# Kernel tuning notes

Hardware: AMD Instinct MI355X
Metric: run time of the kernel (lower is better)

Reference implementation:

```python
import jax, jax.numpy as jnp
import numpy as np

N, P, F, E = 4096, 512, 4096, 65536
FN, FE = 32, 32
H, C = 4, 64
D = H * C
HL = 64
LMAX, LFMAX = 256, 16


def _bn(x, g, b):
    m = x.mean(0)
    v = jnp.mean((x - m) ** 2, 0)
    return (x - m) / jnp.sqrt(v + 1e-5) * g + b


def _gat(x, src, dst, eattr, W, We, asrc, adst, aedge, bias):
    # PyG GATConv with edge_dim: self-loops appended with fill_value='mean' edge attrs
    n = x.shape[0]
    cnt = jax.ops.segment_sum(jnp.ones((eattr.shape[0],), eattr.dtype), dst, n)
    sums = jax.ops.segment_sum(eattr, dst, n)
    loop_attr = jnp.where(cnt[:, None] > 0, sums / jnp.maximum(cnt, 1.0)[:, None], 0.0)
    loops = jnp.arange(n, dtype=src.dtype)
    s2 = jnp.concatenate([src, loops])
    d2 = jnp.concatenate([dst, loops])
    ea = jnp.concatenate([eattr, loop_attr], 0)
    h = (x @ W).reshape(n, H, C)
    e = (ea @ We).reshape(-1, H, C)
    logits = jax.nn.leaky_relu((h * asrc).sum(-1)[s2] + (h * adst).sum(-1)[d2] + (e * aedge).sum(-1), 0.2)
    mx = jax.ops.segment_max(logits, d2, n)
    w = jnp.exp(logits - mx[d2])
    alpha = w / jax.ops.segment_sum(w, d2, n)[d2]  # softmax over incoming edges per dst
    out = jax.ops.segment_sum(h[s2] * alpha[:, :, None], d2, n).reshape(n, D) + bias
    return out, s2, d2, alpha


def _lstm(seq, Wih, Whh, bih, bhh):
    # torch single-layer batch_first LSTM; gate order i,f,g,o
    B = seq.shape[0]
    hid = Whh.shape[1]
    def step(carry, xt):
        hp, cp = carry
        z = xt @ Wih.T + hp @ Whh.T + bih + bhh
        i, f, g, o = jnp.split(z, 4, axis=-1)
        c = jax.nn.sigmoid(f) * cp + jax.nn.sigmoid(i) * jnp.tanh(g)
        hh = jax.nn.sigmoid(o) * jnp.tanh(c)
        return (hh, c), hh
    init = (jnp.zeros((B, hid), seq.dtype), jnp.zeros((B, hid), seq.dtype))
    _, ys = jax.lax.scan(step, init, seq.transpose(1, 0, 2))
    return ys.transpose(1, 0, 2)


def _pack(x, mask_f, max_len):
    # scatter node ids into [S, max_len] slots (cumsum positions), then gather x
    mask = mask_f > 0.5
    n, S = mask.shape
    lengths = mask.sum(0)
    pos = jnp.cumsum(mask, 0) - 1
    slot = jnp.where(mask, jnp.arange(S)[None, :] * max_len + pos, S * max_len)
    node_ids = jnp.broadcast_to(jnp.arange(n, dtype=jnp.int32)[:, None], (n, S))
    buf = jnp.zeros(S * max_len + 1, jnp.int32).at[slot.reshape(-1)].set(node_ids.reshape(-1))
    nfs = buf[: S * max_len].reshape(S, max_len)
    valid = jnp.arange(max_len)[None, :] < lengths[:, None]
    seq = jnp.where(valid[:, :, None], x[nfs], 0.0)
    return seq, lengths


def _node_seq(x, mask_f, max_len, Wih, Whh, bih, bhh):
    seq, lengths = _pack(x, mask_f, max_len)
    out = _lstm(seq, Wih, Whh, bih, bhh)
    return out[jnp.arange(seq.shape[0]), lengths - 1]


def _splice(x, src_f, snk_f, emap, alpha, max_len, Wih, Whh, bih, bhh):
    # pair k-th source True with k-th sink True in row-major flatten order (torch masked-select semantics)
    src_m = src_f > 0.5
    snk_m = snk_f > 0.5
    n, S = src_m.shape
    lengths = src_m.sum(0)
    pos = jnp.cumsum(src_m, 0) - 1
    node_ids = jnp.broadcast_to(jnp.arange(n, dtype=jnp.int32)[:, None], (n, S)).reshape(-1)
    srcf = src_m.reshape(-1)
    snkf = snk_m.reshape(-1)
    total = n * S
    rank_snk = jnp.cumsum(snkf) - 1
    snk_by_rank = jnp.zeros(total + 1, jnp.int32).at[jnp.where(snkf, rank_snk, total)].set(node_ids)
    paired = snk_by_rank[jnp.cumsum(srcf) - 1]
    slot = jnp.where(src_m, jnp.arange(S)[None, :] * max_len + pos, S * max_len).reshape(-1)
    sbuf = jnp.zeros(S * max_len + 1, jnp.int32).at[slot].set(node_ids)
    tbuf = jnp.zeros(S * max_len + 1, jnp.int32).at[slot].set(paired)
    sn = sbuf[: S * max_len].reshape(S, max_len)
    tn = tbuf[: S * max_len].reshape(S, max_len)
    att = alpha[emap[sn * n + tn]]  # [S, T, H]
    se = (x[sn].reshape(S, max_len, H, C) * att[..., None]).reshape(S, max_len, D)
    te = (x[tn].reshape(S, max_len, H, C) * att[..., None]).reshape(S, max_len, D)
    emb = jnp.concatenate([se, te], -1)
    valid = jnp.arange(max_len)[None, :] < lengths[:, None]
    emb = jnp.where(valid[:, :, None], emb, 0.0)
    out = _lstm(emb, Wih, Whh, bih, bhh)
    return out[jnp.arange(S), lengths - 1]


def _compat(paths, frags):
    # mismatch-count reformulation of ((path==frag) | ~span_mask).all(0): exact for 0/1 masks
    n = paths.shape[0]
    relevance = (paths.T @ frags) > 0.0
    fb = frags > 0.5
    fs = jnp.argmax(fb, 0)
    fe = n - 1 - jnp.argmax(fb[::-1], 0)
    r = jnp.arange(n)[:, None]
    fmask = ((r >= fs[None, :]) & (r <= fe[None, :])).astype(paths.dtype)
    mism = frags.T @ (1.0 - paths) + (fmask - frags).T @ paths  # [F, P]
    compat = mism.T == 0.0
    pos = (relevance & compat).astype(paths.dtype)
    neg = (relevance & (~compat)).astype(paths.dtype)
    return pos, neg


def reference(x, edge_index, edge_attr, candidate_paths, candidate_paths_source, candidate_paths_sink, path_abundance, fragments, bn_x_g, bn_x_b, bn_e_g, bn_e_b, gat0_W, gat0_We, gat0_asrc, gat0_adst, gat0_aedge, gat0_bias, gat1_W, gat1_We, gat1_asrc, gat1_adst, gat1_aedge, gat1_bias, node_Wih, node_Whh, node_bih, node_bhh, splice_Wih, splice_Whh, splice_bih, splice_bhh, frag_Wih, frag_Whh, frag_bih, frag_bhh, fc1_W, fc1_b, fc2_W, fc2_b):
    xn = _bn(x, bn_x_g, bn_x_b)
    ea = _bn(edge_attr, bn_e_g, bn_e_b)
    src, dst = edge_index[0], edge_index[1]
    h, _, _, _ = _gat(xn, src, dst, ea, gat0_W, gat0_We, gat0_asrc, gat0_adst, gat0_aedge, gat0_bias)
    h = jax.nn.elu(h)
    h, s2, d2, alpha = _gat(h, src, dst, ea, gat1_W, gat1_We, gat1_asrc, gat1_adst, gat1_aedge, gat1_bias)
    h = jax.nn.elu(h)
    n = h.shape[0]
    emap = jnp.zeros(n * n, jnp.int32).at[s2 * n + d2].set(jnp.arange(s2.shape[0], dtype=jnp.int32))
    node_emb = _node_seq(h, candidate_paths, LMAX, node_Wih, node_Whh, node_bih, node_bhh)
    splice_emb = _splice(h, candidate_paths_source, candidate_paths_sink, emap, alpha, LMAX, splice_Wih, splice_Whh, splice_bih, splice_bhh)
    path_emb = jnp.concatenate([node_emb, splice_emb, path_abundance[:, None]], -1)
    frag_emb = _node_seq(h, fragments, LFMAX, frag_Wih, frag_Whh, frag_bih, frag_bhh)
    pos, neg = _compat(candidate_paths, fragments)
    combined = jnp.concatenate([path_emb, pos @ frag_emb, neg @ frag_emb], -1)
    score = jax.nn.relu(combined @ fc1_W.T + fc1_b) @ fc2_W.T + fc2_b
    return jax.nn.sigmoid(score[:, 0])


def setup_inputs():
    rng = np.random.default_rng(0)
    keys = jax.random.split(jax.random.key(0), 40)
    idx = np.arange(N)[:, None]
    ps = rng.integers(0, N - LMAX, P)
    pl = rng.integers(16, LMAX + 1, P)
    cp = ((idx >= ps) & (idx < ps + pl)).astype(np.float32)
    cps = ((idx >= ps) & (idx < ps + pl - 1)).astype(np.float32)
    cpk = ((idx >= ps + 1) & (idx < ps + pl)).astype(np.float32)
    fst = rng.integers(0, N - LFMAX, F)
    fl = rng.integers(2, LFMAX + 1, F)
    fr = ((idx >= fst) & (idx < fst + fl)).astype(np.float32)
    # unique off-diagonal edges; first N-1 are consecutive (n, n+1) so splice lookups hit real edges
    consec = np.arange(N - 1) * (N - 1) + np.arange(N - 1)
    r_rand = rng.choice(N * (N - 1), size=E, replace=False)
    r = np.concatenate([consec, np.setdiff1d(r_rand, consec)])[:E]
    esrc = r // (N - 1)
    rem = r % (N - 1)
    edst = rem + (rem >= esrc)
    edge_index = jnp.asarray(np.stack([esrc, edst]).astype(np.int32))
    g = lambda k, s, sc=0.1: jax.random.normal(keys[k], s, jnp.float32) * sc
    return dict(
        x=g(0, (N, FN), 1.0),
        edge_index=edge_index,
        edge_attr=g(1, (E, FE), 1.0),
        candidate_paths=jnp.asarray(cp),
        candidate_paths_source=jnp.asarray(cps),
        candidate_paths_sink=jnp.asarray(cpk),
        path_abundance=jax.random.uniform(keys[2], (P,)),
        fragments=jnp.asarray(fr),
        bn_x_g=jnp.ones((FN,)), bn_x_b=jnp.zeros((FN,)),
        bn_e_g=jnp.ones((FE,)), bn_e_b=jnp.zeros((FE,)),
        gat0_W=g(3, (FN, D)), gat0_We=g(4, (FE, D)), gat0_asrc=g(5, (H, C)), gat0_adst=g(6, (H, C)), gat0_aedge=g(7, (H, C)), gat0_bias=g(8, (D,)),
        gat1_W=g(9, (D, D)), gat1_We=g(10, (FE, D)), gat1_asrc=g(11, (H, C)), gat1_adst=g(12, (H, C)), gat1_aedge=g(13, (H, C)), gat1_bias=g(14, (D,)),
        node_Wih=g(15, (4 * HL, D)), node_Whh=g(16, (4 * HL, HL)), node_bih=g(17, (4 * HL,)), node_bhh=g(18, (4 * HL,)),
        splice_Wih=g(19, (4 * HL, 2 * D)), splice_Whh=g(20, (4 * HL, HL)), splice_bih=g(21, (4 * HL,)), splice_bhh=g(22, (4 * HL,)),
        frag_Wih=g(23, (4 * HL, D)), frag_Whh=g(24, (4 * HL, HL)), frag_bih=g(25, (4 * HL,)), frag_bhh=g(26, (4 * HL,)),
        fc1_W=g(27, (HL, 4 * HL + 1)), fc1_b=g(28, (HL,)), fc2_W=g(29, (1, HL)), fc2_b=g(30, (1,)),
    )
```

## Files before the change

### kernel.cpp

```cpp
#include <hip/hip_runtime.h>


constexpr int cN = 4096, cP = 512, cE = 65536, cF = 4096, cM = cE + cN;
constexpr int cLMAX = 256;

typedef float f32x4 __attribute__((ext_vector_type(4)));
typedef unsigned int u32;
typedef u32 u32x4 __attribute__((ext_vector_type(4)));

#define DEV __device__ __forceinline__
DEV float sigf(float x)  { return 1.f / (1.f + __expf(-x)); }
DEV float tanhx(float x) { return 2.f / (1.f + __expf(-2.f * x)) - 1.f; }
DEV float eluf(float x)  { return x > 0.f ? x : (__expf(x) - 1.f); }
DEV float lrelu(float x) { return x > 0.f ? x : 0.2f * x; }
DEV u32   b16rne(float f){ u32 u = __float_as_uint(f); u += 0x7fff + ((u >> 16) & 1); return u >> 16; }
DEV float lobf(u32 d)    { return __uint_as_float(d << 16); }
DEV float hibf(u32 d)    { return __uint_as_float(d & 0xffff0000u); }

#define LBAR() asm volatile("s_waitcnt lgkmcnt(0)\n\ts_barrier" ::: "memory")


DEV void dev_bn_stats(const float* __restrict__ x, long rows,
                      float* sums, float* sumsq, int bid, int nb,
                      float* ls, float* lq) {
  int tid = threadIdx.x;
  long total = rows * 32;
  float s = 0.f, q = 0.f;
  for (long i = (long)bid * 256 + tid; i < total; i += (long)nb * 256) {
    float v = x[i]; s += v; q += v * v;
  }
  ls[tid] = s; lq[tid] = q; __syncthreads();
  if (tid < 32) {
    float S = 0.f, Q = 0.f;
    for (int j = tid; j < 256; j += 32) { S += ls[j]; Q += lq[j]; }
    atomicAdd(&sums[tid], S); atomicAdd(&sumsq[tid], Q);
  }
}

DEV void dev_prep_small(const float* We0, const float* ae0,
                        const float* We1, const float* ae1,
                        const float* nbih, const float* nbhh,
                        const float* fbih, const float* fbhh,
                        const float* sbih, const float* sbhh,
                        float* q0, float* q1, float* nbo, float* fbo, float* sbo) {
  int tid = threadIdx.x;
  if (tid < 128) {
    int k = tid >> 2, hh = tid & 3;
    float s0 = 0.f, s1 = 0.f;
    for (int c = 0; c < 64; c++) {
      s0 += We0[k * 256 + hh * 64 + c] * ae0[hh * 64 + c];
      s1 += We1[k * 256 + hh * 64 + c] * ae1[hh * 64 + c];
    }
    q0[tid] = s0; q1[tid] = s1;
  }
  nbo[tid] = nbih[tid] + nbhh[tid];
  fbo[tid] = fbih[tid] + fbhh[tid];
  sbo[tid] = sbih[tid] + sbhh[tid];
}

DEV void dev_pack(const float* WN, const float* WS, const float* WF,
                  u32* pN, u32* pS, u32* pF, int bid) {
  int gid = bid * 256 + threadIdx.x;
  int mat = gid >> 13, idx = gid & 8191;
  const float* w = (mat == 0) ? WN : (mat == 1 ? WS : WF);
  u32* d = (mat == 0) ? pN : (mat == 1 ? pS : pF);
  float a = w[idx * 2], b = w[idx * 2 + 1];
  d[idx] = b16rne(a) | (b16rne(b) << 16);
}

DEV void dev_deg_count(const int* __restrict__ ei, int* deg, int bid) {
  int m = bid * 256 + threadIdx.x;
  if (m < cE) atomicAdd(&deg[ei[cE + m]], 1);
}

DEV void dev_bn_apply(const float* __restrict__ x, const float* __restrict__ e,
                      const float* bnst, const float* xg, const float* xb,
                      const float* eg, const float* eb,
                      float* xn, float* ea, int bid, int nb, float* sc) {
  int tid = threadIdx.x;
  if (tid < 32) {
    float m = bnst[tid] / (float)cN;
    float v = bnst[32 + tid] / (float)cN - m * m;
    float s = xg[tid] * rsqrtf(v + 1e-5f);
    sc[tid] = s; sc[32 + tid] = xb[tid] - m * s;
  } else if (tid < 64) {
    int c = tid - 32;
    float m = bnst[64 + c] / (float)cE;
    float v = bnst[96 + c] / (float)cE - m * m;
    float s = eg[c] * rsqrtf(v + 1e-5f);
    sc[64 + c] = s; sc[96 + c] = eb[c] - m * s;
  }
  __syncthreads();
  long t1 = (long)cN * 32, t2 = t1 + (long)cE * 32;
  for (long i = (long)bid * 256 + tid; i < t2; i += (long)nb * 256) {
    if (i < t1) { int c = (int)(i & 31); xn[i] = x[i] * sc[c] + sc[32 + c]; }
    else { long j = i - t1; int c = (int)(j & 31); ea[j] = e[j] * sc[64 + c] + sc[96 + c]; }
  }
}

DEV void dev_scan_offsets(const int* __restrict__ deg, int* offs,
                          int* tsum, int* tpre) {
  int tid = threadIdx.x;
  int base = tid * 16, s = 0; int loc[16];
  for (int i = 0; i < 16; i++) { loc[i] = s; s += deg[base + i] + 1; }
  tsum[tid] = s; __syncthreads();
  if (tid == 0) { int r = 0; for (int j = 0; j < 256; j++) { tpre[j] = r; r += tsum[j]; } tpre[256] = r; }
  __syncthreads();
  for (int i = 0; i < 16; i++) offs[base + i] = tpre[tid] + loc[i];
  if (tid == 255) offs[cN] = tpre[256];
}

DEV void dev_intervals(const float* __restrict__ cp, const float* __restrict__ cps,
                       const float* __restrict__ fr,
                       int* p_s, int* p_e, int* s_s, int* s_e,
                       int* f_s, int* f_e, int bid, int nb) {
  const long T1 = (long)cN * cP, T2 = 2 * T1, T3 = T2 + (long)cN * cF;
  for (long i = (long)bid * 256 + threadIdx.x; i < T3; i += (long)nb * 256) {
    if (i < T1) {
      if (cp[i] > 0.5f) { int col = (int)(i % cP), row = (int)(i / cP);
        atomicMin(&p_s[col], row); atomicMax(&p_e[col], row); }
    } else if (i < T2) {
      long j = i - T1;
      if (cps[j] > 0.5f) { int col = (int)(j % cP), row = (int)(j / cP);
        atomicMin(&s_s[col], row); atomicMax(&s_e[col], row); }
    } else {
      long j = i - T2;
      if (fr[j] > 0.5f) { int col = (int)(j % cF), row = (int)(j / cF);
        atomicMin(&f_s[col], row); atomicMax(&f_e[col], row); }
    }
  }
}

DEV void dev_csr_fill(const int* __restrict__ ei, const int* __restrict__ offs,
                      int* cursor, int* eids, int bid) {
  int m = bid * 256 + threadIdx.x;
  if (m < cE) {
    int d = ei[cE + m];
    int pos = atomicAdd(&cursor[d], 1);
    eids[offs[d] + pos] = m;
  } else if (m < cM) {
    int n = m - cE;
    int pos = atomicAdd(&cursor[n], 1);
    eids[offs[n] + pos] = m;
  }
}

DEV void dev_loop_attr(const float* __restrict__ ea, const int* __restrict__ offs,
                       const int* __restrict__ eids,
                       const float* q0, const float* q1,
                       float* es0, float* es1, int n, float* la) {
  int tid = threadIdx.x;
  int o0 = offs[n], o1 = offs[n + 1];
  if (tid < 32) {
    float s = 0.f; int cnt = 0;
    for (int x = o0; x < o1; x++) {
      int eid = eids[x];
      if (eid < cE) { s += ea[(size_t)eid * 32 + tid]; cnt++; }
    }
    la[tid] = cnt > 0 ? s / (float)cnt : 0.f;
  }
  __syncthreads();
  if (tid < 8) {
    int hh = tid & 3;
    const float* q = (tid < 4) ? q0 : q1;
    float s = 0.f;
    for (int k = 0; k < 32; k++) s += la[k] * q[k * 4 + hh];
    ((tid < 4) ? es0 : es1)[(size_t)(cE + n) * 4 + hh] = s;
  }
}

DEV void dev_node_scores(const float* __restrict__ h, const float* __restrict__ asrc,
                         const float* __restrict__ adst, float* ssrc, float* sdst,
                         int bid) {
  int idx = bid * 256 + threadIdx.x;
  if (idx >= cN * 4) return;
  int n = idx >> 2, hh = idx & 3;
  float s1 = 0.f, s2 = 0.f;
  const float* hr = h + (size_t)n * 256 + hh * 64;
  const float* a1 = asrc + hh * 64;
  const float* a2 = adst + hh * 64;
  for (int c = 0; c < 64; c++) { float v = hr[c]; s1 += v * a1[c]; s2 += v * a2[c]; }
  ssrc[idx] = s1; sdst[idx] = s2;
}

DEV void dev_es_edges(const float* __restrict__ ea, const float* __restrict__ q,
                      float* es, int bid) {
  int m = bid * 256 + threadIdx.x;
  if (m >= cE) return;
  float a0 = 0.f, a1 = 0.f, a2 = 0.f, a3 = 0.f;
  const float4* r4 = (const float4*)(ea + (size_t)m * 32);
#pragma unroll
  for (int k4 = 0; k4 < 8; k4++) {
    float4 v = r4[k4];
    int k = k4 * 4;
    a0 += v.x * q[k * 4] + v.y * q[(k + 1) * 4] + v.z * q[(k + 2) * 4] + v.w * q[(k + 3) * 4];
    a1 += v.x * q[k * 4 + 1] + v.y * q[(k + 1) * 4 + 1] + v.z * q[(k + 2) * 4 + 1] + v.w * q[(k + 3) * 4 + 1];
    a2 += v.x * q[k * 4 + 2] + v.y * q[(k + 1) * 4 + 2] + v.z * q[(k + 2) * 4 + 2] + v.w * q[(k + 3) * 4 + 2];
    a3 += v.x * q[k * 4 + 3] + v.y * q[(k + 1) * 4 + 3] + v.z * q[(k + 2) * 4 + 3] + v.w * q[(k + 3) * 4 + 3];
  }
  float* o = es + (size_t)m * 4;
  o[0] = a0; o[1] = a1; o[2] = a2; o[3] = a3;
}

template <bool NT, bool PERM>
DEV void dev_gemm(const float* __restrict__ A, const float* __restrict__ B,
                  const float* __restrict__ bias, float* __restrict__ C,
                  int M, int Nc, int K, int lda, int ldb, int ldc,
                  int bid, float (*As)[68], float (*Bs)[68]) {
  int nb = Nc / 64;
  int bx = bid % nb, by = bid / nb;
  int j0 = bx * 64, i0 = by * 64;
  int tid = threadIdx.x, tx = tid % 16, ty = tid / 16;
  float acc[4][4] = {};

  float ar[4], br[4];
  auto loadA = [&](int k0, float* r4) {
#pragma unroll
    for (int p = 0; p < 4; p++) {
      int l = p * 256 + tid; int r = l >> 4, c = l & 15;
      r4[p] = A[(size_t)(i0 + r) * lda + k0 + c];
    }
  };
  auto loadB = [&](int k0, float* r4) {
    if (NT) {
#pragma unroll
      for (int p = 0; p < 4; p++) {
        int l = p * 256 + tid; int r = l >> 4, c = l & 15;
        r4[p] = B[(size_t)(j0 + r) * ldb + k0 + c];
      }
    } else {
#pragma unroll
      for (int p = 0; p < 4; p++) {
        int l = p * 256 + tid; int j = l & 63, c = l >> 6;
        r4[p] = B[(size_t)(k0 + c) * ldb + j0 + j];
      }
    }
  };

  loadA(0, ar); loadB(0, br);
  for (int k0 = 0; k0 < K; k0 += 16) {
#pragma unroll
    for (int p = 0; p < 4; p++) {
      int l = p * 256 + tid;
      As[l & 15][l >> 4] = ar[p];
    }
    if (NT) {
#pragma unroll
      for (int p = 0; p < 4; p++) {
        int l = p * 256 + tid;
        Bs[l & 15][l >> 4] = br[p];
      }
    } else {
#pragma unroll
      for (int p = 0; p < 4; p++) {
        int l = p * 256 + tid;
        Bs[l >> 6][l & 63] = br[p];
      }
    }
    __syncthreads();
    if (k0 + 16 < K) { loadA(k0 + 16, ar); loadB(k0 + 16, br); }
#pragma unroll
    for (int kk = 0; kk < 16; kk++) {
      f32x4 a4 = *(const f32x4*)&As[kk][ty * 4];
      f32x4 b4 = *(const f32x4*)&Bs[kk][tx * 4];
      float av[4] = {a4.x, a4.y, a4.z, a4.w};
      float bv[4] = {b4.x, b4.y, b4.z, b4.w};
#pragma unroll
      for (int u = 0; u < 4; u++)
#pragma unroll
        for (int v = 0; v < 4; v++) acc[u][v] = fmaf(av[u], bv[v], acc[u][v]);
    }
    __syncthreads();
  }
#pragma unroll
  for (int u = 0; u < 4; u++)
#pragma unroll
    for (int v = 0; v < 4; v++) {
      int i = i0 + ty * 4 + u, j = j0 + tx * 4 + v;
      float r = acc[u][v] + (bias ? bias[j] : 0.f);
      int jj = PERM ? (((j & 63) << 2) | (j >> 6)) : j;
      C[(size_t)i * ldc + jj] = r;
    }
}

DEV void dev_gemm_g(const float* __restrict__ hf, const float* __restrict__ sWih,
                    float* __restrict__ Gp, int bid,
                    float (*As)[68], float (*Bs)[68]) {
  int hh = bid & 3, jt = (bid >> 2) & 3, mt = bid >> 4;
  int i0 = mt * 64, j0 = jt * 64;
  int tid = threadIdx.x, tx = tid & 15, ty = tid >> 4;
  float acc[4][4] = {};

  float ar[4], br[4];
  auto loadT = [&](int k0, float* ra, float* rb) {
    int second = (k0 >= 64);
    int kb = hh * 64 + (k0 & 63);
#pragma unroll
    for (int p = 0; p < 4; p++) {
      int l = p * 256 + tid; int r = l >> 4, c = l & 15;
      int row = i0 + r + second;
      ra[p] = (row < cN) ? hf[(size_t)row * 256 + kb + c] : 0.f;
      rb[p] = sWih[(size_t)(j0 + r) * 512 + second * 256 + kb + c];
    }
  };

  loadT(0, ar, br);
  for (int k0 = 0; k0 < 128; k0 += 16) {
#pragma unroll
    for (int p = 0; p < 4; p++) {
      int l = p * 256 + tid;
      As[l & 15][l >> 4] = ar[p];
      Bs[l & 15][l >> 4] = br[p];
    }
    __syncthreads();
    if (k0 + 16 < 128) loadT(k0 + 16, ar, br);
#pragma unroll
    for (int kk = 0; kk < 16; kk++) {
      f32x4 a4 = *(const f32x4*)&As[kk][ty * 4];
      f32x4 b4 = *(const f32x4*)&Bs[kk][tx * 4];
      float av[4] = {a4.x, a4.y, a4.z, a4.w};
      float bv[4] = {b4.x, b4.y, b4.z, b4.w};
#pragma unroll
      for (int u = 0; u < 4; u++)
#pragma unroll
        for (int v = 0; v < 4; v++) acc[u][v] = fmaf(av[u], bv[v], acc[u][v]);
    }
    __syncthreads();
  }
#pragma unroll
  for (int u = 0; u < 4; u++)
#pragma unroll
    for (int v = 0; v < 4; v++) {
      int i = i0 + ty * 4 + u, j = j0 + tx * 4 + v;
      int g = j >> 6, un = j & 63;
      Gp[(size_t)i * 1024 + un * 16 + g * 4 + hh] = acc[u][v];
    }
}

DEV void dev_att_prep(const int* __restrict__ s_s, const int* __restrict__ s_e,
                      const int* __restrict__ offs, const int* __restrict__ eids,
                      const int* __restrict__ ei, const float* __restrict__ alpha1,
                      float* att, int bid) {
  int idx = bid * 256 + threadIdx.x;
  int s = idx / cLMAX, t = idx % cLMAX;
  int ss = s_s[s], len = s_e[s] - ss + 1;
  float4 a4 = make_float4(0.f, 0.f, 0.f, 0.f);
  if (t < len) {
    int a = ss + t, b = a + 1;
    int found = 0;
    for (int x = offs[b]; x < offs[b + 1]; x++) {
      int eid = eids[x];
      int src = (eid < cE) ? ei[eid] : b;
      if (src == a) { found = eid; break; }
    }
    a4 = *(const float4*)&alpha1[(size_t)found * 4];
  }
  *(float4*)&att[(size_t)idx * 4] = a4;
}


__global__ void init_k(float* bnst, int* deg, int* cursor,
                       int* p_s, int* p_e, int* s_s, int* s_e,
                       int* f_s, int* f_e) {
  int i = blockIdx.x * 256 + threadIdx.x;
  if (i < 128) bnst[i] = 0.f;
  if (i < cN) { deg[i] = 0; cursor[i] = 0; f_s[i] = 0x7fffffff; f_e[i] = -1; }
  if (i < cP) { p_s[i] = 0x7fffffff; p_e[i] = -1; s_s[i] = 0x7fffffff; s_e[i] = -1; }
}

__global__ __launch_bounds__(256) void setup_k(
    const float* x, const float* eattr, const int* ei,
    const float* We0, const float* ae0, const float* We1, const float* ae1,
    const float* nbih, const float* nbhh, const float* fbih, const float* fbhh,
    const float* sbih, const float* sbhh,
    const float* WhhN, const float* WhhS, const float* WhhF,
    float* bnst, int* deg,
    float* q0, float* q1, float* nbo, float* fbo, float* sbo,
    u32* pN, u32* pS, u32* pF) {
  __shared__ float ls[256], lq[256];
  int b = blockIdx.x;
  if (b < 64)        dev_bn_stats(x, cN, bnst, bnst + 32, b, 64, ls, lq);
  else if (b < 320)  dev_bn_stats(eattr, cE, bnst + 64, bnst + 96, b - 64, 256, ls, lq);
  else if (b < 576)  dev_deg_count(ei, deg, b - 320);
  else if (b == 576) dev_prep_small(We0, ae0, We1, ae1, nbih, nbhh, fbih, fbhh,
                                    sbih, sbhh, q0, q1, nbo, fbo, sbo);
  else               dev_pack(WhhN, WhhS, WhhF, pN, pS, pF, b - 577);
}

__global__ __launch_bounds__(256) void mid_k(
    const float* x, const float* eattr, const float* bnst,
    const float* xg, const float* xb, const float* eg, const float* eb,
    float* xn, float* ea, const int* deg, int* offs,
    const float* cp, const float* cps, const float* fr,
    int* p_s, int* p_e, int* s_s, int* s_e, int* f_s, int* f_e) {
  __shared__ int ts[256], tp[257];
  int b = blockIdx.x;
  if (b < 2048)       dev_bn_apply(x, eattr, bnst, xg, xb, eg, eb, xn, ea, b, 2048, (float*)ts);
  else if (b == 2048) dev_scan_offsets(deg, offs, ts, tp);
  else                dev_intervals(cp, cps, fr, p_s, p_e, s_s, s_e, f_s, f_e, b - 2049, 4096);
}

__global__ __launch_bounds__(256) void k3(
    const float* xn, const float* g0W, float* h0,
    const int* ei, const int* offs, int* cursor, int* eids) {
  __shared__ __align__(16) float As[16][68], Bs[16][68];
  int b = blockIdx.x;
  if (b < 256) dev_gemm<false, false>(xn, g0W, nullptr, h0, 4096, 256, 32, 32, 256, 256, b, As, Bs);
  else         dev_csr_fill(ei, offs, cursor, eids, b - 256);
}

__global__ __launch_bounds__(256) void k4(
    const float* ea, const int* offs, const int* eids,
    const float* q0, const float* q1, float* es0, float* es1,
    const float* h0, const float* g0as, const float* g0ad,
    float* ssrc0, float* sdst0) {
  __shared__ float la[32];
  int b = blockIdx.x;
  if (b < 4096)      dev_loop_attr(ea, offs, eids, q0, q1, es0, es1, b, la);
  else if (b < 4160) dev_node_scores(h0, g0as, g0ad, ssrc0, sdst0, b - 4096);
  else               dev_es_edges(ea, q0, es0, b - 4160);
}

__global__ __launch_bounds__(256) void gat_agg(
    const float* __restrict__ hfeat, const float* __restrict__ ssrc,
    const float* __restrict__ sdst, const float* __restrict__ es,
    const int* __restrict__ offs, const int* __restrict__ eids,
    const int* __restrict__ ei, const float* __restrict__ bias,
    float* __restrict__ out, float* alpha_out) {
  int n = blockIdx.x, tid = threadIdx.x;
  __shared__ float l_lds[1024 * 4];
  __shared__ int s_lds[1024];
  __shared__ float red[4];
  int o0 = offs[n], o1 = offs[n + 1];
  int deg = o1 - o0; if (deg > 1024) deg = 1024;
  for (int idx = tid; idx < deg * 4; idx += 256) {
    int e = idx >> 2, hh = idx & 3;
    int eid = eids[o0 + e];
    int src = (eid < cE) ? ei[eid] : n;
    if (hh == 0) s_lds[e] = src;
    float lg = ssrc[src * 4 + hh] + sdst[n * 4 + hh] + es[(size_t)eid * 4 + hh];
    l_lds[idx] = lrelu(lg);
  }
  __syncthreads();
  if (tid < 4) {
    float mx = -1e30f;
    for (int e = 0; e < deg; e++) mx = fmaxf(mx, l_lds[e * 4 + tid]);
    float sm = 0.f;
    for (int e = 0; e < deg; e++) {
      float w = __expf(l_lds[e * 4 + tid] - mx);
      l_lds[e * 4 + tid] = w; sm += w;
    }
    red[tid] = 1.f / sm;
  }
  __syncthreads();
  for (int idx = tid; idx < deg * 4; idx += 256) {
    int e = idx >> 2, hh = idx & 3;
    float a = l_lds[idx] * red[hh];
    l_lds[idx] = a;
    if (alpha_out) { int eid = eids[o0 + e]; alpha_out[(size_t)eid * 4 + hh] = a; }
  }
  __syncthreads();
  int c = tid, hh = c >> 6;
  float acc = 0.f;
  for (int e = 0; e < deg; e++)
    acc = fmaf(l_lds[e * 4 + hh], hfeat[(size_t)s_lds[e] * 256 + c], acc);
  acc += bias[c];
  out[(size_t)n * 256 + c] = eluf(acc);
}

__global__ __launch_bounds__(256) void k6(const float* h0e, const float* g1W, float* h1) {
  __shared__ __align__(16) float As[16][68], Bs[16][68];
  dev_gemm<false, false>(h0e, g1W, nullptr, h1, 4096, 256, 256, 256, 256, 256, blockIdx.x, As, Bs);
}

__global__ __launch_bounds__(256) void k7(
    const float* h1, const float* g1as, const float* g1ad,
    float* ssrc1, float* sdst1, const float* ea, const float* q1, float* es1) {
  int b = blockIdx.x;
  if (b < 64) dev_node_scores(h1, g1as, g1ad, ssrc1, sdst1, b);
  else        dev_es_edges(ea, q1, es1, b - 64);
}

__global__ __launch_bounds__(256) void k9(
    const float* hf, const float* nWih, const float* nbo, float* Znp,
    const float* fWih, const float* fbo, float* Zfp,
    const float* sWih, float* Gp,
    const int* s_s, const int* s_e, const int* offs, const int* eids,
    const int* ei, const float* alpha1, float* att) {
  __shared__ __align__(16) float As[16][68], Bs[16][68];
  int b = blockIdx.x;
  if (b < 256)       dev_gemm<true, true>(hf, nWih, nbo, Znp, 4096, 256, 256, 256, 256, 256, b, As, Bs);
  else if (b < 512)  dev_gemm<true, true>(hf, fWih, fbo, Zfp, 4096, 256, 256, 256, 256, 256, b - 256, As, Bs);
  else if (b < 1536) dev_gemm_g(hf, sWih, Gp, b - 512, As, Bs);
  else               dev_att_prep(s_s, s_e, offs, eids, ei, alpha1, att, b - 1536);
}

__global__ __launch_bounds__(256, 4) void lstm_all(
    const float* __restrict__ Znp, const float* __restrict__ Zfp,
    const float* __restrict__ Gp, const float* __restrict__ att,
    const u32* __restrict__ wpN, const u32* __restrict__ wpS,
    const u32* __restrict__ wpF, const float* __restrict__ sbias,
    const int* __restrict__ p_s, const int* __restrict__ p_e,
    const int* __restrict__ s_s, const int* __restrict__ s_e,
    const int* __restrict__ f_s, const int* __restrict__ f_e,
    float* node_emb, float* spl_emb, float* frag_emb) {
  int b = blockIdx.x;
  int tid = threadIdx.x;
  int w = tid >> 6, lane = tid & 63;
  int g = lane & 3, ul = lane >> 2;
  int unit = w * 16 + ul;
  int role, sid;
  if (b < cP) { role = 0; sid = b; }
  else if (b < 2 * cP) { role = 1; sid = b - cP; }
  else { role = 2; sid = b - 2 * cP; }

  const u32* wp = (role == 0) ? wpN : (role == 1 ? wpS : wpF);
  const u32* wrow = wp + (size_t)(g * 64 + unit) * 32;
  u32 wd[32];
#pragma unroll
  for (int j = 0; j < 8; j++) {
    u32x4 v = *(const u32x4*)(wrow + 4 * j);
    wd[4 * j] = v.x; wd[4 * j + 1] = v.y; wd[4 * j + 2] = v.z; wd[4 * j + 3] = v.w;
  }
#pragma unroll
  for (int j = 0; j < 32; j++) asm volatile("" : "+v"(wd[j]));

  int start, len;
  if (role == 0) { start = p_s[sid]; len = p_e[sid] - start + 1; }
  else if (role == 1) { start = s_s[sid]; len = s_e[sid] - start + 1; }
  else { start = f_s[sid]; len = f_e[sid] - start + 1; }

  float sb = (role == 1) ? sbias[g * 64 + unit] : 0.f;

  const float* Zb = (role == 0) ? Znp : Zfp;
  __shared__ float hbuf[2][64];
  if (tid < 64) hbuf[0][tid] = 0.f;
  float cc = 0.f, h = 0.f;

  float zc = 0.f; f32x4 gc = {0.f, 0.f, 0.f, 0.f}, atc = gc;
  if (role == 1) {
    gc = *(const f32x4*)(Gp + (size_t)start * 1024 + tid * 4);
    atc = *(const f32x4*)(att + (size_t)sid * cLMAX * 4);
  } else {
    zc = Zb[(size_t)start * 256 + tid];
  }
  LBAR();

  for (int t = 0; t < len; t++) {
    int rb = t & 1;
    float zin = (role == 1)
        ? sb + atc.x * gc.x + atc.y * gc.y + atc.z * gc.z + atc.w * gc.w
        : zc;

    float znx = zc; f32x4 gnx = gc, atn = atc;
    if (t + 1 < len) {
      if (role == 1) {
        gnx = *(const f32x4*)(Gp + (size_t)(start + t + 1) * 1024 + tid * 4);
        atn = *(const f32x4*)(att + (size_t)(sid * cLMAX + t + 1) * 4);
      } else {
        znx = Zb[(size_t)(start + t + 1) * 256 + tid];
      }
    }

    float za = zin, zb2 = 0.f;
#pragma unroll
    for (int kc = 0; kc < 8; kc++) {
      f32x4 hv = *(const f32x4*)&hbuf[rb][4 * kc];
      u32 d0 = wd[2 * kc], d1 = wd[2 * kc + 1];
      za = fmaf(hv.x, lobf(d0), za); za = fmaf(hv.y, hibf(d0), za);
      za = fmaf(hv.z, lobf(d1), za); za = fmaf(hv.w, hibf(d1), za);
    }
#pragma unroll
    for (int kc = 8; kc < 16; kc++) {
      f32x4 hv = *(const f32x4*)&hbuf[rb][4 * kc];
      u32 d0 = wd[2 * kc], d1 = wd[2 * kc + 1];
      zb2 = fmaf(hv.x, lobf(d0), zb2); zb2 = fmaf(hv.y, hibf(d0), zb2);
      zb2 = fmaf(hv.z, lobf(d1), zb2); zb2 = fmaf(hv.w, hibf(d1), zb2);
    }
    float z = za + zb2;

    int base = lane & ~3;
    float zi = __shfl(z, base, 64);
    float zf = __shfl(z, base + 1, 64);
    float zg = __shfl(z, base + 2, 64);
    float zo = __shfl(z, base + 3, 64);

    float gi = sigf(zi), gf = sigf(zf), gg = tanhx(zg), go = sigf(zo);
    cc = gf * cc + gi * gg;
    h = go * tanhx(cc);

    if (g == 0) hbuf[rb ^ 1][unit] = h;
    LBAR();

    zc = znx; gc = gnx; atc = atn;
  }

  float* dst = (role == 0) ? node_emb : (role == 1 ? spl_emb : frag_emb);
  if (g == 0) dst[(size_t)sid * 64 + unit] = h;
}

__global__ __launch_bounds__(256) void score_final(
    const float* __restrict__ femb, const int* __restrict__ p_s,
    const int* __restrict__ p_e, const int* __restrict__ f_s,
    const int* __restrict__ f_e, const float* __restrict__ nemb,
    const float* __restrict__ semb, const float* __restrict__ abund,
    const float* __restrict__ fc1W, const float* __restrict__ fc1b,
    const float* __restrict__ fc2W, const float* __restrict__ fc2b,
    float* out) {
  int p = blockIdx.x, tid = threadIdx.x;
  __shared__ float cmb[257];
  __shared__ float accp[256], accn[256], r1[64];
  int ps = p_s[p], pe = p_e[p];
  int d = tid & 63, g = tid >> 6;
  float ap = 0.f, an = 0.f;
  for (int f = g; f < cF; f += 4) {
    int fs = f_s[f], fe = f_e[f];
    if (fs <= pe && fe >= ps) {
      float v = femb[(size_t)f * 64 + d];
      if (fs >= ps && fe <= pe) ap += v;
      else an += v;
    }
  }
  accp[tid] = ap; accn[tid] = an; __syncthreads();
  if (tid < 64) {
    cmb[tid] = nemb[(size_t)p * 64 + tid];
    cmb[64 + tid] = semb[(size_t)p * 64 + tid];
    cmb[129 + tid] = accp[tid] + accp[tid + 64] + accp[tid + 128] + accp[tid + 192];
    cmb[193 + tid] = accn[tid] + accn[tid + 64] + accn[tid + 128] + accn[tid + 192];
    if (tid == 0) cmb[128] = abund[p];
  }
  __syncthreads();
  if (tid < 64) {
    float s = fc1b[tid];
    for (int k = 0; k < 257; k++) s = fmaf(cmb[k], fc1W[tid * 257 + k], s);
    r1[tid] = s > 0.f ? s : 0.f;
  }
  __syncthreads();
  if (tid == 0) {
    float s = fc2b[0];
    for (int j = 0; j < 64; j++) s = fmaf(r1[j], fc2W[j], s);
    out[p] = 1.f / (1.f + __expf(-s));
  }
}

extern "C" void kernel_launch(void* const* d_in, const int* in_sizes, int n_in,
                              void* d_out, int out_size, void* d_ws, size_t ws_size,
                              hipStream_t stream) {
  (void)in_sizes; (void)n_in; (void)out_size; (void)ws_size;
  const float* x     = (const float*)d_in[0];
  const int*   ei    = (const int*)  d_in[1];
  const float* eattr = (const float*)d_in[2];
  const float* cp    = (const float*)d_in[3];
  const float* cps   = (const float*)d_in[4];
  const float* abund = (const float*)d_in[6];
  const float* frg   = (const float*)d_in[7];
  const float* bnxg  = (const float*)d_in[8];
  const float* bnxb  = (const float*)d_in[9];
  const float* bneg  = (const float*)d_in[10];
  const float* bneb  = (const float*)d_in[11];
  const float* g0W   = (const float*)d_in[12];
  const float* g0We  = (const float*)d_in[13];
  const float* g0as  = (const float*)d_in[14];
  const float* g0ad  = (const float*)d_in[15];
  const float* g0ae  = (const float*)d_in[16];
  const float* g0b   = (const float*)d_in[17];
  const float* g1W   = (const float*)d_in[18];
  const float* g1We  = (const float*)d_in[19];
  const float* g1as  = (const float*)d_in[20];
  const float* g1ad  = (const float*)d_in[21];
  const float* g1ae  = (const float*)d_in[22];
  const float* g1b   = (const float*)d_in[23];
  const float* nWih  = (const float*)d_in[24];
  const float* nWhh  = (const float*)d_in[25];
  const float* nbih  = (const float*)d_in[26];
  const float* nbhh  = (const float*)d_in[27];
  const float* sWih  = (const float*)d_in[28];
  const float* sWhh  = (const float*)d_in[29];
  const float* sbih  = (const float*)d_in[30];
  const float* sbhh  = (const float*)d_in[31];
  const float* fWih  = (const float*)d_in[32];
  const float* fWhh  = (const float*)d_in[33];
  const float* fbih  = (const float*)d_in[34];
  const float* fbhh  = (const float*)d_in[35];
  const float* fc1W  = (const float*)d_in[36];
  const float* fc1b  = (const float*)d_in[37];
  const float* fc2W  = (const float*)d_in[38];
  const float* fc2b  = (const float*)d_in[39];
  float* out = (float*)d_out;

  char* base = (char*)d_ws;
  size_t used = 0;
  auto alloc = [&](size_t nbytes) -> char* {
    char* p = base + used;
    used += (nbytes + 255) & ~(size_t)255;
    return p;
  };
  float* bnst   = (float*)alloc(128 * 4);
  float* q0     = (float*)alloc(128 * 4);
  float* q1     = (float*)alloc(128 * 4);
  float* nbo    = (float*)alloc(256 * 4);
  float* fbo    = (float*)alloc(256 * 4);
  float* sbo    = (float*)alloc(256 * 4);
  u32*   wpN    = (u32*)alloc(8192 * 4);
  u32*   wpS    = (u32*)alloc(8192 * 4);
  u32*   wpF    = (u32*)alloc(8192 * 4);
  float* xn     = (float*)alloc((size_t)cN * 32 * 4);
  float* eab    = (float*)alloc((size_t)cE * 32 * 4);
  float* h0     = (float*)alloc((size_t)cN * 256 * 4);
  float* h0e    = (float*)alloc((size_t)cN * 256 * 4);
  float* h1     = (float*)alloc((size_t)cN * 256 * 4);
  float* hf     = (float*)alloc((size_t)cN * 256 * 4);
  float* ssrc0  = (float*)alloc((size_t)cN * 4 * 4);
  float* sdst0  = (float*)alloc((size_t)cN * 4 * 4);
  float* ssrc1  = (float*)alloc((size_t)cN * 4 * 4);
  float* sdst1  = (float*)alloc((size_t)cN * 4 * 4);
  float* es0    = (float*)alloc((size_t)cM * 4 * 4);
  float* es1    = (float*)alloc((size_t)cM * 4 * 4);
  float* alpha1 = (float*)alloc((size_t)cM * 4 * 4);
  float* Znp    = (float*)alloc((size_t)cN * 256 * 4);
  float* Zfp    = (float*)alloc((size_t)cN * 256 * 4);
  float* Gp     = (float*)alloc((size_t)cN * 1024 * 4);
  float* attb   = (float*)alloc((size_t)cP * cLMAX * 4 * 4);
  float* nemb   = (float*)alloc((size_t)cP * 64 * 4);
  float* semb   = (float*)alloc((size_t)cP * 64 * 4);
  float* femb   = (float*)alloc((size_t)cF * 64 * 4);
  int* deg    = (int*)alloc(cN * 4);
  int* cursor = (int*)alloc(cN * 4);
  int* offs   = (int*)alloc((cN + 1) * 4);
  int* eidsA  = (int*)alloc(cM * 4);
  int* p_s = (int*)alloc(cP * 4); int* p_e = (int*)alloc(cP * 4);
  int* s_s = (int*)alloc(cP * 4); int* s_e = (int*)alloc(cP * 4);
  int* f_s = (int*)alloc(cF * 4); int* f_e = (int*)alloc(cF * 4);

  init_k<<<16, 256, 0, stream>>>(bnst, deg, cursor, p_s, p_e, s_s, s_e, f_s, f_e);

  setup_k<<<673, 256, 0, stream>>>(x, eattr, ei, g0We, g0ae, g1We, g1ae,
      nbih, nbhh, fbih, fbhh, sbih, sbhh, nWhh, sWhh, fWhh,
      bnst, deg, q0, q1, nbo, fbo, sbo, wpN, wpS, wpF);

  mid_k<<<6145, 256, 0, stream>>>(x, eattr, bnst, bnxg, bnxb, bneg, bneb,
      xn, eab, deg, offs, cp, cps, frg, p_s, p_e, s_s, s_e, f_s, f_e);

  k3<<<528, 256, 0, stream>>>(xn, g0W, h0, ei, offs, cursor, eidsA);

  k4<<<4416, 256, 0, stream>>>(eab, offs, eidsA, q0, q1, es0, es1,
      h0, g0as, g0ad, ssrc0, sdst0);

  gat_agg<<<cN, 256, 0, stream>>>(h0, ssrc0, sdst0, es0, offs, eidsA, ei, g0b, h0e, nullptr);

  k6<<<256, 256, 0, stream>>>(h0e, g1W, h1);

  k7<<<320, 256, 0, stream>>>(h1, g1as, g1ad, ssrc1, sdst1, eab, q1, es1);

  gat_agg<<<cN, 256, 0, stream>>>(h1, ssrc1, sdst1, es1, offs, eidsA, ei, g1b, hf, alpha1);

  k9<<<2048, 256, 0, stream>>>(hf, nWih, nbo, Znp, fWih, fbo, Zfp, sWih, Gp,
      s_s, s_e, offs, eidsA, ei, alpha1, attb);

  lstm_all<<<2 * cP + cF, 256, 0, stream>>>(Znp, Zfp, Gp, attb, wpN, wpS, wpF, sbo,
      p_s, p_e, s_s, s_e, f_s, f_e, nemb, semb, femb);

  score_final<<<cP, 256, 0, stream>>>(femb, p_s, p_e, f_s, f_e, nemb, semb, abund,
      fc1W, fc1b, fc2W, fc2b, out);
}
```

Baseline: 671.3 us.

## Stage LSTM recurrent weights in LDS instead of registers

The LSTM kernel no longer keeps each thread's 32 packed bf16 recurrent weight words in VGPRs. It copies the whole 8192-word weight matrix into shared memory, transposed so each thread reads one 16-byte vector per k-chunk, and reads it every timestep. The launch-bounds occupancy hint is dropped. This cuts register pressure but adds 8 LDS vector loads per step on the serial recurrence path and 32KB of LDS per block, which may limit blocks per CU.

```diff
diff --git a/kernel.cpp b/kernel.cpp
--- a/kernel.cpp
+++ b/kernel.cpp
@@ -495,7 +495,7 @@
   else               dev_att_prep(s_s, s_e, offs, eids, ei, alpha1, att, b - 1536);
 }
 
-__global__ __launch_bounds__(256, 4) void lstm_all(
+__global__ __launch_bounds__(256) void lstm_all(
     const float* __restrict__ Znp, const float* __restrict__ Zfp,
     const float* __restrict__ Gp, const float* __restrict__ att,
     const u32* __restrict__ wpN, const u32* __restrict__ wpS,
@@ -509,32 +509,34 @@
   int w = tid >> 6, lane = tid & 63;
   int g = lane & 3, ul = lane >> 2;
   int unit = w * 16 + ul;
+  int row = g * 64 + unit;
   int role, sid;
   if (b < cP) { role = 0; sid = b; }
   else if (b < 2 * cP) { role = 1; sid = b - cP; }
   else { role = 2; sid = b - 2 * cP; }
 
   const u32* wp = (role == 0) ? wpN : (role == 1 ? wpS : wpF);
-  const u32* wrow = wp + (size_t)(g * 64 + unit) * 32;
-  u32 wd[32];
-#pragma unroll
-  for (int j = 0; j < 8; j++) {
-    u32x4 v = *(const u32x4*)(wrow + 4 * j);
-    wd[4 * j] = v.x; wd[4 * j + 1] = v.y; wd[4 * j + 2] = v.z; wd[4 * j + 3] = v.w;
-  }
-#pragma unroll
-  for (int j = 0; j < 32; j++) asm volatile("" : "+v"(wd[j]));
+
+  __shared__ u32 Wl[8192];
+  __shared__ float hbuf[2][64];
+
+#pragma unroll
+  for (int i = 0; i < 32; i++) {
+    int gidx = i * 256 + tid;
+    u32 v = wp[gidx];
+    int r = gidx >> 5, k2 = gidx & 31;
+    Wl[((k2 >> 2) << 10) + (r << 2) + (k2 & 3)] = v;
+  }
+  if (tid < 64) hbuf[0][tid] = 0.f;
 
   int start, len;
   if (role == 0) { start = p_s[sid]; len = p_e[sid] - start + 1; }
   else if (role == 1) { start = s_s[sid]; len = s_e[sid] - start + 1; }
   else { start = f_s[sid]; len = f_e[sid] - start + 1; }
 
-  float sb = (role == 1) ? sbias[g * 64 + unit] : 0.f;
+  float sb = (role == 1) ? sbias[row] : 0.f;
 
   const float* Zb = (role == 0) ? Znp : Zfp;
-  __shared__ float hbuf[2][64];
-  if (tid < 64) hbuf[0][tid] = 0.f;
   float cc = 0.f, h = 0.f;
 
   float zc = 0.f; f32x4 gc = {0.f, 0.f, 0.f, 0.f}, atc = gc;
@@ -544,7 +546,9 @@
   } else {
     zc = Zb[(size_t)start * 256 + tid];
   }
-  LBAR();
+  __syncthreads();
+
+  const u32* wbase = &Wl[row << 2];
 
   for (int t = 0; t < len; t++) {
     int rb = t & 1;
@@ -564,18 +568,14 @@
 
     float za = zin, zb2 = 0.f;
 #pragma unroll
-    for (int kc = 0; kc < 8; kc++) {
-      f32x4 hv = *(const f32x4*)&hbuf[rb][4 * kc];
-      u32 d0 = wd[2 * kc], d1 = wd[2 * kc + 1];
-      za = fmaf(hv.x, lobf(d0), za); za = fmaf(hv.y, hibf(d0), za);
-      za = fmaf(hv.z, lobf(d1), za); za = fmaf(hv.w, hibf(d1), za);
-    }
-#pragma unroll
-    for (int kc = 8; kc < 16; kc++) {
-      f32x4 hv = *(const f32x4*)&hbuf[rb][4 * kc];
-      u32 d0 = wd[2 * kc], d1 = wd[2 * kc + 1];
-      zb2 = fmaf(hv.x, lobf(d0), zb2); zb2 = fmaf(hv.y, hibf(d0), zb2);
-      zb2 = fmaf(hv.z, lobf(d1), zb2); zb2 = fmaf(hv.w, hibf(d1), zb2);
+    for (int k8 = 0; k8 < 8; k8++) {
+      u32x4 wq = *(const u32x4*)&wbase[k8 << 10];
+      f32x4 h0 = *(const f32x4*)&hbuf[rb][8 * k8];
+      f32x4 h1 = *(const f32x4*)&hbuf[rb][8 * k8 + 4];
+      za  = fmaf(h0.x, lobf(wq.x), za);  za  = fmaf(h0.y, hibf(wq.x), za);
+      za  = fmaf(h0.z, lobf(wq.y), za);  za  = fmaf(h0.w, hibf(wq.y), za);
+      zb2 = fmaf(h1.x, lobf(wq.z), zb2); zb2 = fmaf(h1.y, hibf(wq.z), zb2);
+      zb2 = fmaf(h1.z, lobf(wq.w), zb2); zb2 = fmaf(h1.w, hibf(wq.w), zb2);
     }
     float z = za + zb2;
 
```

New measurement: 826.6 us. 23.1% more time.
